# Performance work log

Measured on AMD Instinct MI355X. Metric: run time of the kernel, lower is better.

Reference implementation:

```python
import jax, jax.numpy as jnp
import numpy as np

B = 2_000_000
EPS = 1e-7


def _skew(v):
    # v: [..., 3] -> [..., 3, 3] skew-symmetric
    z = jnp.zeros_like(v[..., 0])
    return jnp.stack([
        jnp.stack([z, -v[..., 2], v[..., 1]], axis=-1),
        jnp.stack([v[..., 2], z, -v[..., 0]], axis=-1),
        jnp.stack([-v[..., 1], v[..., 0], z], axis=-1),
    ], axis=-2)


def _rodrigues(phi):
    # axis-angle [..., 3] -> rotation matrix [..., 3, 3]
    angle = jnp.linalg.norm(phi, axis=-1, keepdims=True)
    axis = phi / jnp.maximum(angle, 1e-12)
    K = _skew(axis)
    a = angle[..., None]
    I = jnp.eye(3, dtype=phi.dtype)
    return I + jnp.sin(a) * K + (1.0 - jnp.cos(a)) * (K @ K)


def setup_inputs() -> dict:
    key = jax.random.key(0)
    k1, k2, k3 = jax.random.split(key, 3)
    # random rotations via exp-map of random axis-angle vectors
    phi_est = jax.random.normal(k1, (B, 3), dtype=jnp.float32) * 0.8
    phi_tgt = jax.random.normal(k2, (B, 3), dtype=jnp.float32) * 0.8
    C_est = _rodrigues(phi_est)
    C_target = _rodrigues(phi_tgt)
    # SPD information matrices: A A^T + I  (logdet well-defined)
    A = 0.3 * jax.random.normal(k3, (B, 3, 3), dtype=jnp.float32)
    Rinv = jnp.einsum('bij,bkj->bik', A, A) + jnp.eye(3, dtype=jnp.float32)
    return {"C_est": C_est, "C_target": C_target, "Rinv": Rinv}


def so3_log(C):
    # batched SO(3) log map -> [..., 3]
    tr = C[..., 0, 0] + C[..., 1, 1] + C[..., 2, 2]
    cos_angle = jnp.clip(0.5 * (tr - 1.0), -1.0 + EPS, 1.0 - EPS)
    angle = jnp.arccos(cos_angle)
    sin_angle = jnp.sin(angle)
    # angle/(2 sin angle); small-angle Taylor: 0.5 + angle^2/12
    small = angle < 1e-6
    coef = jnp.where(small, 0.5 + angle * angle / 12.0,
                     0.5 * angle / jnp.where(small, 1.0, sin_angle))
    skew = C - jnp.swapaxes(C, -1, -2)
    vee = jnp.stack([skew[..., 2, 1], skew[..., 0, 2], skew[..., 1, 0]], axis=-1)
    return coef[..., None] * vee


def batch_logdet3(M):
    det = (M[..., 0, 0] * (M[..., 1, 1] * M[..., 2, 2] - M[..., 1, 2] * M[..., 2, 1])
           - M[..., 0, 1] * (M[..., 1, 0] * M[..., 2, 2] - M[..., 1, 2] * M[..., 2, 0])
           + M[..., 0, 2] * (M[..., 1, 0] * M[..., 2, 1] - M[..., 1, 1] * M[..., 2, 0]))
    return jnp.log(det)


def reference(C_est, C_target, Rinv):
    # residual = log(C_est @ C_target^T)  -> [B, 3]
    dC = jnp.einsum('bij,bkj->bik', C_est, C_target)
    residual = so3_log(dC)
    # 0.5 * r^T Rinv r  -> [B]
    weighted = 0.5 * jnp.einsum('bi,bij,bj->b', residual, Rinv, residual)
    nll = weighted - 0.5 * batch_logdet3(Rinv)
    return nll
```

## Files before the change

### kernel.cpp

```cpp
#include <hip/hip_runtime.h>

constexpr int BLK = 256;

__device__ __forceinline__ float mul_rn(float a, float b) {
    float r; asm("v_mul_f32 %0, %1, %2" : "=v"(r) : "v"(a), "v"(b)); return r;
}
__device__ __forceinline__ float add_rn(float a, float b) {
    float r; asm("v_add_f32 %0, %1, %2" : "=v"(r) : "v"(a), "v"(b)); return r;
}
__device__ __forceinline__ float sub_rn(float a, float b) {
    float r; asm("v_sub_f32 %0, %1, %2" : "=v"(r) : "v"(a), "v"(b)); return r;
}
__device__ __forceinline__ float fma_rn(float a, float b, float c) {
    float r; asm("v_fma_f32 %0, %1, %2, %3"
                 : "=v"(r) : "v"(a), "v"(b), "v"(c)); return r;
}

__device__ __forceinline__ float dot3_fma_asc(float a0, float a1, float a2,
                                              float b0, float b1, float b2) {
    return fma_rn(a2, b2, fma_rn(a1, b1, mul_rn(a0, b0)));
}

__device__ __forceinline__ void load9(const float* __restrict__ p, float* d) {
    float4 a, b;
    __builtin_memcpy(&a, p,     16);
    __builtin_memcpy(&b, p + 4, 16);
    float c = p[8];
    d[0] = a.x; d[1] = a.y; d[2] = a.z; d[3] = a.w;
    d[4] = b.x; d[5] = b.y; d[6] = b.z; d[7] = b.w;
    d[8] = c;
}

__global__ __launch_bounds__(BLK, 8) void so3_nll_kernel(
    const float* __restrict__ C_est,
    const float* __restrict__ C_tgt,
    const float* __restrict__ Rinv,
    float* __restrict__ out,
    int B)
{
    const int i_raw = blockIdx.x * BLK + threadIdx.x;
    const int i     = min(i_raw, B - 1);
    const size_t base = (size_t)i * 9;

    float E[9], T[9], R[9];
    load9(C_est + base, E);
    load9(C_tgt + base, T);
    load9(Rinv  + base, R);

    float d00 = dot3_fma_asc(E[0],E[1],E[2], T[0],T[1],T[2]);
    float d11 = dot3_fma_asc(E[3],E[4],E[5], T[3],T[4],T[5]);
    float d22 = dot3_fma_asc(E[6],E[7],E[8], T[6],T[7],T[8]);

    float tr = add_rn(add_rn(d00, d11), d22);
    float ca = 0.5f * sub_rn(tr, 1.0f);
    constexpr float HI = 1.0f - 1e-7f;
    ca = fminf(fmaxf(ca, -HI), HI);
    float angle = acosf(ca);
    float sa    = sinf(angle);
    float coef = (0.5f * angle) / sa;

    float d01 = dot3_fma_asc(E[0],E[1],E[2], T[3],T[4],T[5]);
    float d02 = dot3_fma_asc(E[0],E[1],E[2], T[6],T[7],T[8]);
    float d10 = dot3_fma_asc(E[3],E[4],E[5], T[0],T[1],T[2]);
    float d12 = dot3_fma_asc(E[3],E[4],E[5], T[6],T[7],T[8]);
    float d20 = dot3_fma_asc(E[6],E[7],E[8], T[0],T[1],T[2]);
    float d21 = dot3_fma_asc(E[6],E[7],E[8], T[3],T[4],T[5]);

    float r0 = coef * sub_rn(d21, d12);
    float r1 = coef * sub_rn(d02, d20);
    float r2 = coef * sub_rn(d10, d01);

    float w = 0.5f * (r0 * ((R[0]*r0 + R[1]*r1) + R[2]*r2) +
                      r1 * ((R[3]*r0 + R[4]*r1) + R[5]*r2) +
                      r2 * ((R[6]*r0 + R[7]*r1) + R[8]*r2));

    float det = R[0] * (R[4]*R[8] - R[5]*R[7])
              - R[1] * (R[3]*R[8] - R[5]*R[6])
              + R[2] * (R[3]*R[7] - R[4]*R[6]);

    if (i_raw < B)
        out[i_raw] = w - 0.5f * logf(det);
}

extern "C" void kernel_launch(void* const* d_in, const int* in_sizes, int n_in,
                              void* d_out, int out_size, void* d_ws, size_t ws_size,
                              hipStream_t stream) {
    const float* C_est = (const float*)d_in[0];
    const float* C_tgt = (const float*)d_in[1];
    const float* Rinv  = (const float*)d_in[2];
    float* out = (float*)d_out;

    const int B = in_sizes[0] / 9;
    const int blocks = (B + BLK - 1) / BLK;
    so3_nll_kernel<<<blocks, BLK, 0, stream>>>(C_est, C_tgt, Rinv, out, B);
}
```

Before: 206.5 us.

## Process four elements per thread with aligned float4 loads and stores

Each thread now handles four consecutive elements, so its 36 floats per input are 16-byte aligned and load as nine float4 vectors, and the four results go out as one float4 store. This replaces the earlier mix of misaligned float4 and scalar loads with fully aligned vector transactions, and launch bounds drop to 2 waves per SIMD. The cost is about 108 live floats per thread, so register pressure and occupancy fall. Fewer threads in flight may hide memory latency less well, and each thread's accesses stride 144 bytes apart.

```diff
diff --git a/kernel.cpp b/kernel.cpp
--- a/kernel.cpp
+++ b/kernel.cpp
@@ -21,32 +21,8 @@
     return fma_rn(a2, b2, fma_rn(a1, b1, mul_rn(a0, b0)));
 }
 
-__device__ __forceinline__ void load9(const float* __restrict__ p, float* d) {
-    float4 a, b;
-    __builtin_memcpy(&a, p,     16);
-    __builtin_memcpy(&b, p + 4, 16);
-    float c = p[8];
-    d[0] = a.x; d[1] = a.y; d[2] = a.z; d[3] = a.w;
-    d[4] = b.x; d[5] = b.y; d[6] = b.z; d[7] = b.w;
-    d[8] = c;
-}
-
-__global__ __launch_bounds__(BLK, 8) void so3_nll_kernel(
-    const float* __restrict__ C_est,
-    const float* __restrict__ C_tgt,
-    const float* __restrict__ Rinv,
-    float* __restrict__ out,
-    int B)
-{
-    const int i_raw = blockIdx.x * BLK + threadIdx.x;
-    const int i     = min(i_raw, B - 1);
-    const size_t base = (size_t)i * 9;
-
-    float E[9], T[9], R[9];
-    load9(C_est + base, E);
-    load9(C_tgt + base, T);
-    load9(Rinv  + base, R);
-
+__device__ __forceinline__ float so3_nll_elem(const float* E, const float* T,
+                                              const float* R) {
     float d00 = dot3_fma_asc(E[0],E[1],E[2], T[0],T[1],T[2]);
     float d11 = dot3_fma_asc(E[3],E[4],E[5], T[3],T[4],T[5]);
     float d22 = dot3_fma_asc(E[6],E[7],E[8], T[6],T[7],T[8]);
@@ -78,8 +54,53 @@
               - R[1] * (R[3]*R[8] - R[5]*R[6])
               + R[2] * (R[3]*R[7] - R[4]*R[6]);
 
-    if (i_raw < B)
-        out[i_raw] = w - 0.5f * logf(det);
+    return w - 0.5f * logf(det);
+}
+
+__global__ __launch_bounds__(BLK, 2) void so3_nll_kernel(
+    const float* __restrict__ C_est,
+    const float* __restrict__ C_tgt,
+    const float* __restrict__ Rinv,
+    float* __restrict__ out,
+    int B)
+{
+    const long long nquad_full = (long long)(B >> 2);
+    const long long q = (long long)blockIdx.x * BLK + threadIdx.x;
+
+    if (q < nquad_full) {
+        const float4* gE = reinterpret_cast<const float4*>(C_est) + q * 9;
+        const float4* gT = reinterpret_cast<const float4*>(C_tgt) + q * 9;
+        const float4* gR = reinterpret_cast<const float4*>(Rinv)  + q * 9;
+
+        float e[36], t[36], rr[36];
+        #pragma unroll
+        for (int i = 0; i < 9; ++i) {
+            *reinterpret_cast<float4*>(&e[4 * i])  = gE[i];
+            *reinterpret_cast<float4*>(&t[4 * i])  = gT[i];
+            *reinterpret_cast<float4*>(&rr[4 * i]) = gR[i];
+        }
+
+        float nll[4];
+        #pragma unroll
+        for (int k = 0; k < 4; ++k)
+            nll[k] = so3_nll_elem(&e[9 * k], &t[9 * k], &rr[9 * k]);
+
+        float4 o;
+        o.x = nll[0]; o.y = nll[1]; o.z = nll[2]; o.w = nll[3];
+        *reinterpret_cast<float4*>(out + q * 4) = o;
+    } else if (q == nquad_full) {
+        for (long long el = nquad_full * 4; el < (long long)B; ++el) {
+            float E[9], T[9], R[9];
+            const size_t base = (size_t)el * 9;
+            #pragma unroll
+            for (int j = 0; j < 9; ++j) {
+                E[j] = C_est[base + j];
+                T[j] = C_tgt[base + j];
+                R[j] = Rinv [base + j];
+            }
+            out[el] = so3_nll_elem(E, T, R);
+        }
+    }
 }
 
 extern "C" void kernel_launch(void* const* d_in, const int* in_sizes, int n_in,
@@ -91,6 +112,7 @@
     float* out = (float*)d_out;
 
     const int B = in_sizes[0] / 9;
-    const int blocks = (B + BLK - 1) / BLK;
+    const long long nquad_total = (B >> 2) + ((B & 3) ? 1 : 0);
+    const int blocks = (int)((nquad_total + BLK - 1) / BLK);
     so3_nll_kernel<<<blocks, BLK, 0, stream>>>(C_est, C_tgt, Rinv, out, B);
 }
```

New measurement: 211.3 us. 1.02x slower.
